# Kernel optimization log

Measured on AMD Instinct MI355X. Metric: run time of the kernel, lower is better.

Reference implementation:

```python
import jax, jax.numpy as jnp
import numpy as np

SOFTENING = 1e-6
EPS = 1e-9
CUTOFF = 0.1
K_NEG = 4
MARGIN = 1.0
KE_FACTOR = 1e-3


def setup_inputs() -> dict:
    key = jax.random.key(0)
    ks = jax.random.split(key, 16)
    B, S, D8, W = 4, 2048, 8, 16
    N = B * S
    return {
        "positions_2d": jax.random.normal(ks[0], (B, S, 2), dtype=jnp.float32),
        "masses": jax.random.uniform(ks[1], (B, S, 1), dtype=jnp.float32),
        "vel_2d": jax.random.normal(ks[2], (N, 2), dtype=jnp.float32),
        "pos_8d": jax.random.normal(ks[3], (N, D8), dtype=jnp.float32),
        "pos_pos_2d": jax.random.normal(ks[4], (N, 2), dtype=jnp.float32),
        "pos_pos_8d": jax.random.normal(ks[5], (N, D8), dtype=jnp.float32),
        "positive_masses": jax.random.uniform(ks[6], (N, 1), dtype=jnp.float32),
        "neg_pos_2d": jax.random.normal(ks[7], (N * K_NEG, 2), dtype=jnp.float32),
        "neg_pos_8d": jax.random.normal(ks[8], (N * K_NEG, D8), dtype=jnp.float32),
        "neg_masses": jax.random.uniform(ks[9], (N * K_NEG, 1), dtype=jnp.float32),
        "exp_masses": jax.random.uniform(ks[10], (N * K_NEG, 1), dtype=jnp.float32),
        "G": jnp.float32(1.0),
        "repulsion_strength": jnp.float32(0.5),
        "well_centers": jax.random.normal(ks[11], (W, D8), dtype=jnp.float32),
        "well_strength": jnp.float32(0.1),
        "temperature": jnp.float32(1.0),
        "entropy_coeff": jnp.float32(0.01),
    }


def _calculate_forces(positions_2d, masses, G, repulsion_strength):
    # positions_2d: [B,S,2], masses: [B,S,1]
    B, S, _ = positions_2d.shape
    # diff[b,i,j] = pos[b,j] - pos[b,i]  -> [B,S,S,2]
    diff = positions_2d[:, None, :, :] - positions_2d[:, :, None, :]
    dist_sq = jnp.sum(diff * diff, axis=-1) + SOFTENING  # [B,S,S]
    dist = jnp.sqrt(dist_sq)
    diag = jnp.eye(S, dtype=bool)  # [S,S], broadcasts over B
    dist_safe = jnp.where(diag, 1.0, dist)
    dist_sq_safe = jnp.where(diag, 1.0, dist_sq)
    mm = masses[:, :, None, 0] * masses[:, None, :, 0]  # [B,S,S]
    attractive = jax.nn.relu(G) * mm / dist_sq_safe
    rep_strength = jax.nn.relu(repulsion_strength)
    repulsive = rep_strength * jax.nn.relu(1.0 - dist_safe / CUTOFF) / (dist_sq_safe * dist_safe + EPS)
    total_mag = repulsive - attractive  # [B,S,S]
    force_vectors = total_mag[..., None] * diff / (dist_safe[..., None] + EPS)
    return jnp.sum(force_vectors, axis=2)  # [B,S,2]


def _cdist(a, b):
    # Euclidean cdist: [N,D] x [W,D] -> [N,W]; W=16 so dense is cheap
    d = a[:, None, :] - b[None, :, :]
    return jnp.sqrt(jnp.sum(d * d, axis=-1))


def _grand_unifying_loss(pos_2d, vel_2d, pos_8d, masses_flat, pos_pos_2d, pos_pos_8d,
                         positive_masses, neg_pos_2d, neg_pos_8d, neg_masses, exp_masses,
                         G, well_centers, well_strength, temperature, entropy_coeff):
    Gp = jax.nn.relu(G)
    dist_pos_2d = jnp.linalg.norm(pos_2d - pos_pos_2d, axis=-1) + EPS  # [N]
    pe_pairwise_pos = -Gp * (masses_flat * positive_masses)[:, 0] / dist_pos_2d
    pos_2d_rep = jnp.repeat(pos_2d, K_NEG, axis=0)  # [N*K,2]
    dist_neg_2d = jnp.linalg.norm(pos_2d_rep - neg_pos_2d, axis=-1) + EPS
    pe_pairwise_neg = -Gp * (exp_masses * neg_masses)[:, 0] / dist_neg_2d

    ws = jax.nn.relu(well_strength)
    all_pos_8d = jnp.concatenate([pos_8d, pos_pos_8d], axis=0)  # [2N,8]
    min_dist_pos = jnp.min(_cdist(all_pos_8d, well_centers), axis=1)
    pe_well_pos = ws * min_dist_pos ** 2
    all_neg_8d = jnp.concatenate([jnp.repeat(pos_8d, K_NEG, axis=0), neg_pos_8d], axis=0)
    min_dist_neg = jnp.min(_cdist(all_neg_8d, well_centers), axis=1)
    pe_well_neg = ws * min_dist_neg ** 2

    U_pos = jnp.mean(pe_pairwise_pos) + jnp.mean(pe_well_pos)
    U_neg = jnp.mean(pe_pairwise_neg) + jnp.mean(pe_well_neg)
    batch_variance = jnp.mean(jnp.var(all_pos_8d, axis=0, ddof=1))  # torch.var is unbiased
    entropy_term = jax.nn.relu(temperature) * jax.nn.relu(entropy_coeff) * batch_variance
    F_pos = U_pos - entropy_term
    F_neg = U_neg - entropy_term
    free_energy_loss = jax.nn.relu(MARGIN + F_pos - F_neg)
    # Original: mean(masses[N,1] * ke[N]) broadcasts to an [N,N] outer product;
    # mean of the outer product == mean(m) * mean(ke) (same value and gradients)
    ke = jnp.sum(vel_2d * vel_2d, axis=-1)  # [N]
    ke_loss = KE_FACTOR * 0.5 * jnp.mean(masses_flat) * jnp.mean(ke)
    return free_energy_loss + ke_loss


def reference(positions_2d, masses, vel_2d, pos_8d, pos_pos_2d, pos_pos_8d,
              positive_masses, neg_pos_2d, neg_pos_8d, neg_masses, exp_masses,
              G, repulsion_strength, well_centers, well_strength, temperature, entropy_coeff):
    forces = _calculate_forces(positions_2d, masses, G, repulsion_strength)
    pos_flat = positions_2d.reshape(-1, 2)
    masses_flat = masses.reshape(-1, 1)
    loss = _grand_unifying_loss(pos_flat, vel_2d, pos_8d, masses_flat, pos_pos_2d,
                                pos_pos_8d, positive_masses, neg_pos_2d, neg_pos_8d,
                                neg_masses, exp_masses, G, well_centers, well_strength,
                                temperature, entropy_coeff)
    return forces, loss
```

## Files before the change

### kernel.cpp

```cpp
#include <hip/hip_runtime.h>

#define SEQ    2048
#define N_PTS  8192
#define NK     32768
#define N2     16384
#define NACC   22
#define NLOSSBLK 256
#define SLOT_DOUBLES (NLOSSBLK * NACC)
#define CTR_OFFSET   (SLOT_DOUBLES * 8)

__device__ __forceinline__ float frcp(float x)  { return __builtin_amdgcn_rcpf(x); }
__device__ __forceinline__ float fsqrt_(float x){ return __builtin_amdgcn_sqrtf(x); }

__device__ __forceinline__ float min_dist2(float4 a, float4 b, const float* __restrict__ wc)
{
    float best = 3.4e38f;
    #pragma unroll
    for (int w = 0; w < 16; ++w) {
        const float* c = &wc[w * 8];
        float d, s;
        d = a.x - c[0]; s = d * d;
        d = a.y - c[1]; s = fmaf(d, d, s);
        d = a.z - c[2]; s = fmaf(d, d, s);
        d = a.w - c[3]; s = fmaf(d, d, s);
        d = b.x - c[4]; s = fmaf(d, d, s);
        d = b.y - c[5]; s = fmaf(d, d, s);
        d = b.z - c[6]; s = fmaf(d, d, s);
        d = b.w - c[7]; s = fmaf(d, d, s);
        best = fminf(best, s);
    }
    return best;
}

__global__ __launch_bounds__(256) void fused_kernel(
    const float* __restrict__ pos,
    const float* __restrict__ mass,
    const float* __restrict__ vel,
    const float* __restrict__ pos8,
    const float* __restrict__ pp2,
    const float* __restrict__ pp8,
    const float* __restrict__ pmass,
    const float* __restrict__ negp2,
    const float* __restrict__ negp8,
    const float* __restrict__ negm,
    const float* __restrict__ expm,
    const float* __restrict__ Gptr,
    const float* __restrict__ Rptr,
    const float* __restrict__ wellc,
    const float* __restrict__ wstr,
    const float* __restrict__ tPtr,
    const float* __restrict__ ecPtr,
    float* __restrict__ out,
    double* __restrict__ slots,
    unsigned int* __restrict__ ctr)
{
    const int tid = threadIdx.x;
    const int blk = blockIdx.x;

    if (blk < 256) {
        __shared__ float sx[SEQ], sy[SEQ], sm[SEQ];
        __shared__ float rf[2][8][32];

        const int b  = blk >> 6;
        const int it = blk & 63;
        const int rowbase = b * SEQ;

        const float2* p2 = (const float2*)pos;
        for (int k = tid; k < SEQ; k += 256) {
            const float2 v = p2[rowbase + k];
            sx[k] = v.x; sy[k] = v.y;
            sm[k] = mass[rowbase + k];
        }
        const float Gv = fmaxf(Gptr[0], 0.0f);
        const float Rv = fmaxf(Rptr[0], 0.0f);
        __syncthreads();

        const int il = tid & 31;
        const int js = tid >> 5;
        const int iloc = it * 32 + il;
        const float px = sx[iloc];
        const float py = sy[iloc];
        const float ci = Gv * sm[iloc];

        float fx = 0.0f, fy = 0.0f;
        const int j0 = js * 256;
        #pragma unroll 4
        for (int jj = 0; jj < 256; ++jj) {
            const int j = j0 + jj;
            const float dx = sx[j] - px;
            const float dy = sy[j] - py;
            const float r2 = fmaf(dx, dx, fmaf(dy, dy, 1e-6f));
            const float r  = fsqrt_(r2);
            const float rp = r + 1e-9f;
            float mor = -(ci * sm[j]) * frcp(r2 * rp);
            const float t = fmaf(-10.0f, r, 1.0f);
            if (t > 0.0f) {
                mor += (Rv * t) * frcp(fmaf(r2, r, 1e-9f) * rp);
            }
            fx = fmaf(mor, dx, fx);
            fy = fmaf(mor, dy, fy);
        }
        rf[0][js][il] = fx;
        rf[1][js][il] = fy;
        __syncthreads();
        if (tid < 64) {
            const int comp = tid >> 5, i2 = tid & 31;
            float s = 0.0f;
            #pragma unroll
            for (int q = 0; q < 8; ++q) s += rf[comp][q][i2];
            out[(rowbase + it * 32 + i2) * 2 + comp] = s;
        }
        return;
    }

    __shared__ float  wc[128];
    __shared__ double red[4][NACC];
    __shared__ int    lastflag;

    if (tid < 128) wc[tid] = wellc[tid];
    if (tid == 0)  lastflag = 0;
    __syncthreads();

    const int lb  = blk - 256;
    const int idx = lb * 256 + tid;

    double acc[NACC];
    #pragma unroll
    for (int k = 0; k < NACC; ++k) acc[k] = 0.0;

    {
        const float* row = (idx < NK) ? (pos8 + (idx >> 2) * 8)
                                      : (negp8 + (idx - NK) * 8);
        const float4 a = ((const float4*)row)[0];
        const float4 b = ((const float4*)row)[1];
        acc[3] = (double)min_dist2(a, b, wc);
    }
    if (idx < NK) {
        const int i = idx >> 2;
        const float dx = pos[i * 2 + 0] - negp2[idx * 2 + 0];
        const float dy = pos[i * 2 + 1] - negp2[idx * 2 + 1];
        const float d  = fsqrt_(fmaf(dx, dx, dy * dy)) + 1e-9f;
        acc[1] = (double)(expm[idx] * negm[idx] / d);
    }
    if (idx < N2) {
        const float* row = (idx < N_PTS) ? (pos8 + idx * 8)
                                         : (pp8 + (idx - N_PTS) * 8);
        const float4 a = ((const float4*)row)[0];
        const float4 b = ((const float4*)row)[1];
        acc[2] = (double)min_dist2(a, b, wc);
        acc[4]  = (double)a.x;  acc[12] = (double)(a.x * a.x);
        acc[5]  = (double)a.y;  acc[13] = (double)(a.y * a.y);
        acc[6]  = (double)a.z;  acc[14] = (double)(a.z * a.z);
        acc[7]  = (double)a.w;  acc[15] = (double)(a.w * a.w);
        acc[8]  = (double)b.x;  acc[16] = (double)(b.x * b.x);
        acc[9]  = (double)b.y;  acc[17] = (double)(b.y * b.y);
        acc[10] = (double)b.z;  acc[18] = (double)(b.z * b.z);
        acc[11] = (double)b.w;  acc[19] = (double)(b.w * b.w);
    }
    if (idx < N_PTS) {
        const float dx = pos[idx * 2 + 0] - pp2[idx * 2 + 0];
        const float dy = pos[idx * 2 + 1] - pp2[idx * 2 + 1];
        const float d  = fsqrt_(fmaf(dx, dx, dy * dy)) + 1e-9f;
        acc[0]  = (double)(mass[idx] * pmass[idx] / d);
        acc[20] = (double)mass[idx];
        const float vx = vel[idx * 2 + 0];
        const float vy = vel[idx * 2 + 1];
        acc[21] = (double)fmaf(vx, vx, vy * vy);
    }

    const int lane = tid & 63, wid = tid >> 6;
    #pragma unroll
    for (int k = 0; k < NACC; ++k) {
        double v = acc[k];
        for (int off = 32; off > 0; off >>= 1) v += __shfl_down(v, off, 64);
        if (lane == 0) red[wid][k] = v;
    }
    __syncthreads();
    if (tid < NACC) {
        slots[lb * NACC + tid] = red[0][tid] + red[1][tid] + red[2][tid] + red[3][tid];
    }
    __syncthreads();
    if (tid == 0) {
        __threadfence();
        const unsigned int ticket = atomicAdd(ctr, 1u);
        if (ticket == NLOSSBLK - 1) lastflag = 1;
    }
    __syncthreads();
    if (!lastflag) return;

    __threadfence();
    #pragma unroll
    for (int k = 0; k < NACC; ++k) {
        double v = slots[tid * NACC + k];
        for (int off = 32; off > 0; off >>= 1) v += __shfl_down(v, off, 64);
        if (lane == 0) red[wid][k] = v;
    }
    __syncthreads();
    if (tid == 0) {
        double s[NACC];
        #pragma unroll
        for (int k = 0; k < NACC; ++k)
            s[k] = red[0][k] + red[1][k] + red[2][k] + red[3][k];

        const double Gp  = fmax((double)Gptr[0], 0.0);
        const double wsp = fmax((double)wstr[0], 0.0);
        const double T   = fmax((double)tPtr[0], 0.0);
        const double ec  = fmax((double)ecPtr[0], 0.0);
        const double Nd = 8192.0, NKd = 32768.0, N2d = 16384.0, NK2d = 65536.0;

        const double U_pos = -Gp * s[0] / Nd  + wsp * s[2] / N2d;
        const double U_neg = -Gp * s[1] / NKd + wsp * s[3] / NK2d;

        double var = 0.0;
        for (int d = 0; d < 8; ++d) {
            const double sx_ = s[4 + d], sxx = s[12 + d];
            var += (sxx - sx_ * sx_ / N2d) / (N2d - 1.0);
        }
        var *= 0.125;
        const double ent = T * ec * var;
        const double Fp = U_pos - ent, Fn = U_neg - ent;
        double fel = 1.0 + Fp - Fn;
        if (fel < 0.0) fel = 0.0;
        const double ke_loss = 1e-3 * 0.5 * (s[20] / Nd) * (s[21] / Nd);
        out[16384] = (float)(fel + ke_loss);
    }
}

extern "C" void kernel_launch(void* const* d_in, const int* in_sizes, int n_in,
                              void* d_out, int out_size, void* d_ws, size_t ws_size,
                              hipStream_t stream)
{
    const float* pos   = (const float*)d_in[0];
    const float* mass  = (const float*)d_in[1];
    const float* vel   = (const float*)d_in[2];
    const float* pos8  = (const float*)d_in[3];
    const float* pp2   = (const float*)d_in[4];
    const float* pp8   = (const float*)d_in[5];
    const float* pmass = (const float*)d_in[6];
    const float* negp2 = (const float*)d_in[7];
    const float* negp8 = (const float*)d_in[8];
    const float* negm  = (const float*)d_in[9];
    const float* expm  = (const float*)d_in[10];
    const float* Gp    = (const float*)d_in[11];
    const float* Rp    = (const float*)d_in[12];
    const float* wellc = (const float*)d_in[13];
    const float* wstr  = (const float*)d_in[14];
    const float* temp  = (const float*)d_in[15];
    const float* ecoef = (const float*)d_in[16];

    float*        out   = (float*)d_out;
    double*       slots = (double*)d_ws;
    unsigned int* ctr   = (unsigned int*)((char*)d_ws + CTR_OFFSET);

    hipMemsetAsync(ctr, 0, sizeof(unsigned int), stream);

    fused_kernel<<<512, 256, 0, stream>>>(pos, mass, vel, pos8, pp2, pp8, pmass,
                                          negp2, negp8, negm, expm, Gp, Rp,
                                          wellc, wstr, temp, ecoef,
                                          out, slots, ctr);
}
```

Baseline: 109.3 us.

## Double force blocks, pack particle data as float4, and run loss blocks first

```diff
diff --git a/kernel.cpp b/kernel.cpp
--- a/kernel.cpp
+++ b/kernel.cpp
@@ -6,6 +6,7 @@
 #define N2     16384
 #define NACC   22
 #define NLOSSBLK 256
+#define NFORCE   512
 #define SLOT_DOUBLES (NLOSSBLK * NACC)
 #define CTR_OFFSET   (SLOT_DOUBLES * 8)
 
@@ -57,58 +58,75 @@
     const int tid = threadIdx.x;
     const int blk = blockIdx.x;
 
-    if (blk < 256) {
-        __shared__ float sx[SEQ], sy[SEQ], sm[SEQ];
-        __shared__ float rf[2][8][32];
-
-        const int b  = blk >> 6;
-        const int it = blk & 63;
+    if (blk >= NLOSSBLK) {
+        __shared__ float4 s4[SEQ];
+        __shared__ float  rf[2][16][16];
+
+        const int fb = blk - NLOSSBLK;
+        const int b  = fb >> 7;
+        const int it = fb & 127;
         const int rowbase = b * SEQ;
 
         const float2* p2 = (const float2*)pos;
         for (int k = tid; k < SEQ; k += 256) {
             const float2 v = p2[rowbase + k];
-            sx[k] = v.x; sy[k] = v.y;
-            sm[k] = mass[rowbase + k];
+            s4[k] = make_float4(v.x, v.y, mass[rowbase + k], 0.0f);
         }
         const float Gv = fmaxf(Gptr[0], 0.0f);
         const float Rv = fmaxf(Rptr[0], 0.0f);
         __syncthreads();
 
-        const int il = tid & 31;
-        const int js = tid >> 5;
-        const int iloc = it * 32 + il;
-        const float px = sx[iloc];
-        const float py = sy[iloc];
-        const float ci = Gv * sm[iloc];
-
-        float fx = 0.0f, fy = 0.0f;
-        const int j0 = js * 256;
+        const int il = tid & 15;
+        const int js = tid >> 4;
+        const int iloc = it * 16 + il;
+        const float px = s4[iloc].x;
+        const float py = s4[iloc].y;
+        const float ci = Gv * s4[iloc].z;
+
+        float fx0 = 0.0f, fy0 = 0.0f, fx1 = 0.0f, fy1 = 0.0f;
+        const int j0 = js * 128;
         #pragma unroll 4
-        for (int jj = 0; jj < 256; ++jj) {
-            const int j = j0 + jj;
-            const float dx = sx[j] - px;
-            const float dy = sy[j] - py;
-            const float r2 = fmaf(dx, dx, fmaf(dy, dy, 1e-6f));
-            const float r  = fsqrt_(r2);
-            const float rp = r + 1e-9f;
-            float mor = -(ci * sm[j]) * frcp(r2 * rp);
-            const float t = fmaf(-10.0f, r, 1.0f);
-            if (t > 0.0f) {
-                mor += (Rv * t) * frcp(fmaf(r2, r, 1e-9f) * rp);
+        for (int jj = 0; jj < 128; jj += 2) {
+            const float4 q0 = s4[j0 + jj];
+            const float4 q1 = s4[j0 + jj + 1];
+            {
+                const float dx = q0.x - px;
+                const float dy = q0.y - py;
+                const float r2 = fmaf(dx, dx, fmaf(dy, dy, 1e-6f));
+                const float r  = fsqrt_(r2);
+                const float rp = r + 1e-9f;
+                float mor = -(ci * q0.z) * frcp(r2 * rp);
+                const float t = fmaf(-10.0f, r, 1.0f);
+                if (t > 0.0f) {
+                    mor += (Rv * t) * frcp(fmaf(r2, r, 1e-9f) * rp);
+                }
+                fx0 = fmaf(mor, dx, fx0);
+                fy0 = fmaf(mor, dy, fy0);
             }
-            fx = fmaf(mor, dx, fx);
-            fy = fmaf(mor, dy, fy);
-        }
-        rf[0][js][il] = fx;
-        rf[1][js][il] = fy;
+            {
+                const float dx = q1.x - px;
+                const float dy = q1.y - py;
+                const float r2 = fmaf(dx, dx, fmaf(dy, dy, 1e-6f));
+                const float r  = fsqrt_(r2);
+                const float rp = r + 1e-9f;
+                float mor = -(ci * q1.z) * frcp(r2 * rp);
+                const float t = fmaf(-10.0f, r, 1.0f);
+                if (t > 0.0f) {
+                    mor += (Rv * t) * frcp(fmaf(r2, r, 1e-9f) * rp);
+                }
+                fx1 = fmaf(mor, dx, fx1);
+                fy1 = fmaf(mor, dy, fy1);
+            }
+        }
+        rf[0][js][il] = fx0 + fx1;
+        rf[1][js][il] = fy0 + fy1;
         __syncthreads();
-        if (tid < 64) {
-            const int comp = tid >> 5, i2 = tid & 31;
+        if (tid < 32) {
+            const int comp = tid >> 4, i2 = tid & 15;
             float s = 0.0f;
             #pragma unroll
-            for (int q = 0; q < 8; ++q) s += rf[comp][q][i2];
-            out[(rowbase + it * 32 + i2) * 2 + comp] = s;
+            for (int q = 0; q < 16; ++q) s += rf[comp][q][i2];
+            out[(rowbase + it * 16 + i2) * 2 + comp] = s;
         }
         return;
     }
@@ -121,7 +139,7 @@
     if (tid == 0)  lastflag = 0;
     __syncthreads();
 
-    const int lb  = blk - 256;
+    const int lb  = blk;
     const int idx = lb * 256 + tid;
 
     double acc[NACC];
@@ -254,8 +272,8 @@
 
     hipMemsetAsync(ctr, 0, sizeof(unsigned int), stream);
 
-    fused_kernel<<<512, 256, 0, stream>>>(pos, mass, vel, pos8, pp2, pp8, pmass,
-                                          negp2, negp8, negm, expm, Gp, Rp,
-                                          wellc, wstr, temp, ecoef,
+    fused_kernel<<<NLOSSBLK + NFORCE, 256, 0, stream>>>(pos, mass, vel, pos8, pp2,
+                                          pp8, pmass, negp2, negp8, negm, expm,
+                                          Gp, Rp, wellc, wstr, temp, ecoef,
                                           out, slots, ctr);
 }
```

Measured after the change: 111.8 us. 1.02x slower.
